# Kernel optimization log

Measured on AMD Instinct MI355X. Metric: run time of the kernel, lower is better.

Reference implementation:

```python
import jax, jax.numpy as jnp
import numpy as np

B, C, H, W = 16, 256, 56, 56
WH, WW = 7, 7
NH = 8            # heads
HID = 1024        # mlp hidden = int(4*dim)
N = WH * WW
EPS = 1e-5


def _rel_index():
    # mirrors the torch buffer computation in Rel_Attention.__init__
    coords = np.stack(np.meshgrid(np.arange(WH), np.arange(WW), indexing='ij')).reshape(2, -1)  # (2, N)
    rel = coords[:, :, None] - coords[:, None, :]  # (2, N, N)
    rel[0] += WH - 1
    rel[1] += WW - 1
    rel[0] *= 2 * WW - 1
    return jnp.asarray(rel.sum(0).reshape(-1))  # (N*N,)

REL_IDX = _rel_index()


def channel_ln(x, w, b):
    # LayerNorm over channel dim of NCHW tensor (permute -> LN -> permute back)
    xt = x.transpose(0, 2, 3, 1)  # BHWC
    mu = xt.mean(-1, keepdims=True)
    var = xt.var(-1, keepdims=True)
    xt = (xt - mu) / jnp.sqrt(var + EPS) * w + b
    return xt.transpose(0, 3, 1, 2)


def to_blocks(x):
    # (B,C,H,W) -> (B, H/wh, W/ww, C, wh, ww)
    b, c, h, w = x.shape
    x = x.reshape(b, c, h // WH, WH, w // WW, WW)
    return x.transpose(0, 2, 4, 1, 3, 5)


def unblock(x):
    # faithful to original: reshape(B, C, Hb*win_W, Hb*win_W)  (square sizes)
    b, hb, wb, c, wh, ww = x.shape
    return x.transpose(0, 3, 1, 4, 2, 5).reshape(b, c, hb * ww, hb * ww)


def rel_attention(xw, qkv_w, qkv_b, proj_w, proj_b, table):
    b, hb, wb, c = xw.shape[:4]
    hd = c // NH
    scale = hd ** (-0.5)
    xf = xw.reshape(-1, c, N)                                  # (M, C, N)
    qkv = jnp.einsum('oc,mcn->mon', qkv_w, xf) + qkv_b[None, :, None]
    q, k, v = jnp.split(qkv, 3, axis=1)

    def heads(t):
        return t.reshape(-1, NH, hd, N).transpose(0, 1, 3, 2)  # (M, h, N, d)

    q, k, v = heads(q), heads(k), heads(v)
    bias = table[REL_IDX].reshape(N, N, NH).transpose(2, 0, 1)  # (h, N, N)
    attn = jnp.einsum('mhnd,mhkd->mhnk', q, k) * scale + bias
    attn = jax.nn.softmax(attn, axis=-1)
    o = jnp.einsum('mhnk,mhkd->mhnd', attn, v)                 # (M, h, N, d)
    o = o.transpose(0, 1, 3, 2).reshape(-1, c, N)              # (M, C, N)
    o = jnp.einsum('oc,mcn->mon', proj_w, o) + proj_b[None, :, None]
    return o.reshape(b, hb, wb, c, WH, WW)


def mlp(x, fc1_w, fc1_b, fc2_w, fc2_b):
    h = jnp.einsum('oc,bchw->bohw', fc1_w, x) + fc1_b[None, :, None, None]
    h = jax.nn.gelu(h, approximate=False)
    return jnp.einsum('oc,bchw->bohw', fc2_w, h) + fc2_b[None, :, None, None]


def setup_inputs() -> dict:
    key = jax.random.key(0)
    ks = jax.random.split(key, 8)
    s = 0.02
    return {
        'x': jax.random.normal(ks[0], (B, C, H, W), jnp.float32),
        'ln1_w': jnp.ones((C,), jnp.float32),
        'ln1_b': jnp.zeros((C,), jnp.float32),
        'ln2_w': jnp.ones((C,), jnp.float32),
        'ln2_b': jnp.zeros((C,), jnp.float32),
        'qkv_w': jax.random.normal(ks[1], (3 * C, C), jnp.float32) * s,
        'qkv_b': jnp.zeros((3 * C,), jnp.float32),
        'proj_w': jax.random.normal(ks[2], (C, C), jnp.float32) * s,
        'proj_b': jnp.zeros((C,), jnp.float32),
        'rel_bias_table': jax.random.normal(ks[3], ((2 * WH - 1) * (2 * WW - 1), NH), jnp.float32) * s,
        'fc1_w': jax.random.normal(ks[4], (HID, C), jnp.float32) * s,
        'fc1_b': jnp.zeros((HID,), jnp.float32),
        'fc2_w': jax.random.normal(ks[5], (C, HID), jnp.float32) * s,
        'fc2_b': jnp.zeros((C,), jnp.float32),
    }


def reference(x, ln1_w, ln1_b, ln2_w, ln2_b, qkv_w, qkv_b, proj_w, proj_b,
              rel_bias_table, fc1_w, fc1_b, fc2_w, fc2_b):
    out = to_blocks(channel_ln(x, ln1_w, ln1_b))
    out = rel_attention(out, qkv_w, qkv_b, proj_w, proj_b, rel_bias_table)
    # original applies attn a second time before unblocking
    out = rel_attention(out, qkv_w, qkv_b, proj_w, proj_b, rel_bias_table)
    x = x + unblock(out)
    x = x + mlp(channel_ln(x, ln2_w, ln2_b), fc1_w, fc1_b, fc2_w, fc2_b)
    return x
```

## Files before the change

### kernel.cpp

```cpp
#include <hip/hip_runtime.h>
#include <stdint.h>

typedef uint16_t u16;
typedef short bf16x4 __attribute__((ext_vector_type(4)));
typedef short bf16x8 __attribute__((ext_vector_type(8)));
typedef float f32x4 __attribute__((ext_vector_type(4)));

__device__ __forceinline__ float bf2f(u16 s) {
  union { unsigned int i; float f; } c; c.i = ((unsigned int)s) << 16; return c.f;
}
__device__ __forceinline__ u16 f2bf(float f) {
  union { float f; unsigned int i; } c; c.f = f;
  unsigned int u = c.i;
  u += 0x7FFFu + ((u >> 16) & 1u);
  return (u16)(u >> 16);
}
__device__ __forceinline__ f32x4 mfma16(bf16x8 a, bf16x8 b, f32x4 c) {
  return __builtin_amdgcn_mfma_f32_16x16x32_bf16(a, b, c, 0, 0, 0);
}
__device__ __forceinline__ int dtype_flag(const u16* ln1w_raw) { return ln1w_raw[0] == 0x3F80 ? 1 : 0; }
__device__ __forceinline__ float loadF(const void* p, size_t i, int flag) {
  return flag ? bf2f(((const u16*)p)[i]) : ((const float*)p)[i];
}

__device__ __forceinline__ int frag_idx8(int n, int c0, int qc) {
  return (n < 48) ? (((n >> 4) * 8 + c0) * 64 + (n & 15) + 16 * qc)
                  : (1536 + c0 * 4 + qc);
}

#define OFF_QKVW 0
#define OFF_QKVB 196608
#define OFF_PROJW 197376
#define OFF_PROJB 262912
#define OFF_REL 263168
#define OFF_FC1W 264520
#define OFF_FC1B 526664
#define OFF_FC2W 527688
#define OFF_FC2B 789832
#define OFF_LN1W 790088
#define OFF_LN1B 790344
#define OFF_LN2W 790600
#define OFF_LN2B 790856
#define WC_TOTAL 791112

__global__ __launch_bounds__(256) void k_convert(const u16* __restrict__ ln1w_raw,
    const void* qkvw, const void* qkvb, const void* projw, const void* projb,
    const void* rel, const void* fc1w, const void* fc1b, const void* fc2w, const void* fc2b,
    const void* ln1w, const void* ln1b, const void* ln2w, const void* ln2b,
    u16* __restrict__ dst) {
  const int flag = dtype_flag(ln1w_raw);
  int i = blockIdx.x * 256 + threadIdx.x;
  if (i >= WC_TOTAL) return;
  const void* src; int off;
  if      (i < OFF_QKVB)  { src = qkvw;  off = i - OFF_QKVW; }
  else if (i < OFF_PROJW) { src = qkvb;  off = i - OFF_QKVB; }
  else if (i < OFF_PROJB) { src = projw; off = i - OFF_PROJW; }
  else if (i < OFF_REL)   { src = projb; off = i - OFF_PROJB; }
  else if (i < OFF_FC1W)  { src = rel;   off = i - OFF_REL; }
  else if (i < OFF_FC1B)  { src = fc1w;  off = i - OFF_FC1W; }
  else if (i < OFF_FC2W)  { src = fc1b;  off = i - OFF_FC1B; }
  else if (i < OFF_FC2B)  { src = fc2w;  off = i - OFF_FC2W; }
  else if (i < OFF_LN1W)  { src = fc2b;  off = i - OFF_FC2B; }
  else if (i < OFF_LN1B)  { src = ln1w;  off = i - OFF_LN1W; }
  else if (i < OFF_LN2W)  { src = ln1b;  off = i - OFF_LN1B; }
  else if (i < OFF_LN2B)  { src = ln2w;  off = i - OFF_LN2W; }
  else                    { src = ln2b;  off = i - OFF_LN2B; }
  if (i < OFF_QKVB) {
    int j = off & 7, li = (off >> 3) & 63, c0i = (off >> 9) & 7, grp = off >> 12;
    off = (grp * 16 + (li & 15)) * 256 + c0i * 32 + (li >> 4) * 8 + j;
  } else if (i >= OFF_PROJW && i < OFF_PROJB) {
    int j = off & 7, li = (off >> 3) & 63, c0i = (off >> 9) & 7, grp = off >> 12;
    off = (grp * 16 + (li & 15)) * 256 + c0i * 32 + (li >> 4) * 8 + j;
  } else if (i >= OFF_FC1W && i < OFF_FC1B) {
    int j = off & 7, li = (off >> 3) & 63, hj = (off >> 9) & 1, c0i = (off >> 10) & 7,
        w = (off >> 13) & 3, ch = off >> 15;
    off = (ch * 128 + w * 32 + hj * 16 + (li & 15)) * 256 + c0i * 32 + (li >> 4) * 8 + j;
  } else if (i >= OFF_FC2W && i < OFF_FC2B) {
    int j = off & 7, li = (off >> 3) & 63, oct = (off >> 9) & 3, kki = (off >> 11) & 3,
        ch = (off >> 13) & 7, w = off >> 16;
    off = (w * 64 + oct * 16 + (li & 15)) * 1024 + ch * 128 + kki * 32 + (li >> 4) * 8 + j;
  }
  dst[i] = flag ? ((const u16*)src)[off] : f2bf(((const float*)src)[off]);
}

__global__ __launch_bounds__(256) void k_ln1b(const void* __restrict__ xin,
                                              const u16* __restrict__ ln1w_raw,
                                              const u16* __restrict__ lw,
                                              const u16* __restrict__ lb,
                                              u16* __restrict__ win) {
  const int flag = dtype_flag(ln1w_raw);
  __shared__ float tile[56 * 257];
  __shared__ float smu[56], srs[56];
  const int bid = blockIdx.x;
  const int b = bid / 56, h = bid - b * 56;
  const int t = threadIdx.x;
  const int hb = h / 7, ph = h - hb * 7;
  if (!flag) {
#pragma unroll
    for (int i = 0; i < 14; ++i) {
      int chunk = i * 256 + t;
      int c = chunk / 14, w4 = (chunk - c * 14) * 4;
      const float* xp4 = (const float*)xin + ((size_t)(b * 256 + c) * 56 + h) * 56 + w4;
      f32x4 v = *(const f32x4*)xp4;
#pragma unroll
      for (int k = 0; k < 4; ++k) tile[(w4 + k) * 257 + c] = v[k];
    }
  } else {
#pragma unroll
    for (int i = 0; i < 7; ++i) {
      int chunk = i * 256 + t;
      int c = chunk / 7, w8 = (chunk - c * 7) * 8;
      const u16* xp8 = (const u16*)xin + ((size_t)(b * 256 + c) * 56 + h) * 56 + w8;
      bf16x8 v = *(const bf16x8*)xp8;
#pragma unroll
      for (int k = 0; k < 8; ++k) tile[(w8 + k) * 257 + c] = bf2f((u16)v[k]);
    }
  }
  __syncthreads();
  {
    const int row = t >> 2, qq = t & 3;
    float s = 0.f, q = 0.f;
    if (row < 56) {
      const float* tr = &tile[row * 257 + qq];
#pragma unroll 8
      for (int c0 = 0; c0 < 64; ++c0) { float v = tr[c0 * 4]; s += v; q += v * v; }
    }
    s += __shfl_xor(s, 1, 64); q += __shfl_xor(q, 1, 64);
    s += __shfl_xor(s, 2, 64); q += __shfl_xor(q, 2, 64);
    if (row < 56 && qq == 0) {
      float mm = s * (1.f / 256.f);
      float var = q * (1.f / 256.f) - mm * mm;
      smu[row] = mm; srs[row] = rsqrtf(var + 1e-5f);
    }
  }
  __syncthreads();
#pragma unroll
  for (int i = 0; i < 7; ++i) {
    int eid8 = i * 256 + t;
    int wp = eid8 >> 5, c8 = (eid8 & 31) << 3;
    const float mm = smu[wp], rs = srs[wp];
    const int m = b * 64 + hb * 8 + (wp / 7), n = ph * 7 + (wp % 7);
    bf16x8 o;
#pragma unroll
    for (int j = 0; j < 8; ++j) {
      int c = c8 + j;
      o[j] = (short)f2bf((tile[wp * 257 + c] - mm) * rs * bf2f(lw[c]) + bf2f(lb[c]));
    }
    const int idx8 = frag_idx8(n, c8 >> 5, (c8 >> 3) & 3);
    *(bf16x8*)&win[(size_t)m * 12544 + idx8 * 8] = o;
  }
}

__global__ __launch_bounds__(512) void k_attn_stage(const u16* __restrict__ win,
                                                    const u16* __restrict__ qkvw,
                                                    const u16* __restrict__ qkvb,
                                                    const u16* __restrict__ rel,
                                                    const u16* __restrict__ projw,
                                                    const u16* __restrict__ projb,
                                                    u16* __restrict__ wout,
                                                    int out_frag) {
  __shared__ __align__(16) u16 xs[12544];
  __shared__ __align__(16) u16 wa[8][7424];
  const int m = blockIdx.x;
  const int t = threadIdx.x;
  const int w = t >> 6, li = t & 63, lane = li & 15, quad = li >> 4;
  const int hg = w;
  const f32x4 z = {0.f, 0.f, 0.f, 0.f};
  const u16* src = win + (size_t)m * 12544;
#pragma unroll
  for (int i = 0; i < 4; ++i) {
    int chunk = i * 512 + t;
    if (chunk < 1568) *(bf16x8*)&xs[chunk * 8] = *(const bf16x8*)&src[(size_t)chunk * 8];
  }
  u16* qw = wa[w];
  u16* kw = wa[w] + 2560;
  u16* vw = wa[w] + 5120;
  u16* Pw = wa[w];
  u16* Ow = wa[w];
  for (int i = li; i < 15 * 40; i += 64) { qw[49 * 40 + i] = 0; kw[49 * 40 + i] = 0; }
  for (int i = li; i < 32 * 15; i += 64) { int d = i / 15, jn = i - d * 15; vw[d * 72 + 49 + jn] = 0; }
  __syncthreads();
  const float SCALE = 0.17677669529663687f;
  auto xfrag = [&](int nt, int c0i) -> bf16x8 {
    int idx8 = (nt < 3) ? ((nt * 8 + c0i) * 64 + li) : (1536 + c0i * 4 + quad);
    return *(const bf16x8*)&xs[idx8 * 8];
  };
#pragma unroll
  for (int part = 0; part < 2; ++part) {
    const int obase = part * 256 + hg * 32;
    f32x4 acc[4][2];
#pragma unroll
    for (int i = 0; i < 4; ++i) { acc[i][0] = z; acc[i][1] = z; }
#pragma unroll
    for (int c0i = 0; c0i < 8; ++c0i) {
      bf16x8 a[4], b[2];
#pragma unroll
      for (int nt = 0; nt < 4; ++nt) a[nt] = xfrag(nt, c0i);
#pragma unroll
      for (int oj = 0; oj < 2; ++oj)
        b[oj] = *(const bf16x8*)&qkvw[(size_t)(((part * 16 + hg * 2 + oj) * 8 + c0i) * 64 + li) * 8];
      __builtin_amdgcn_s_setprio(1);
#pragma unroll
      for (int nt = 0; nt < 4; ++nt)
#pragma unroll
        for (int oj = 0; oj < 2; ++oj) acc[nt][oj] = mfma16(a[nt], b[oj], acc[nt][oj]);
      __builtin_amdgcn_s_setprio(0);
    }
    u16* dstL = part ? kw : qw;
#pragma unroll
    for (int oj = 0; oj < 2; ++oj) {
      const int d = oj * 16 + lane;
      const float bias = bf2f(qkvb[obase + d]);
#pragma unroll
      for (int nt = 0; nt < 4; ++nt)
#pragma unroll
        for (int r = 0; r < 4; ++r) {
          int n = nt * 16 + quad * 4 + r;
          if (n < 49) dstL[n * 40 + d] = f2bf(acc[nt][oj][r] + bias);
        }
    }
  }
  {
    f32x4 acc[2][4];
#pragma unroll
    for (int i = 0; i < 2; ++i)
#pragma unroll
      for (int j = 0; j < 4; ++j) acc[i][j] = z;
#pragma unroll
    for (int c0i = 0; c0i < 8; ++c0i) {
      bf16x8 a[2], b[4];
#pragma unroll
      for (int vj = 0; vj < 2; ++vj)
        a[vj] = *(const bf16x8*)&qkvw[(size_t)(((32 + hg * 2 + vj) * 8 + c0i) * 64 + li) * 8];
#pragma unroll
      for (int nt = 0; nt < 4; ++nt) b[nt] = xfrag(nt, c0i);
      __builtin_amdgcn_s_setprio(1);
#pragma unroll
      for (int vj = 0; vj < 2; ++vj)
#pragma unroll
        for (int nt = 0; nt < 4; ++nt) acc[vj][nt] = mfma16(a[vj], b[nt], acc[vj][nt]);
      __builtin_amdgcn_s_setprio(0);
    }
#pragma unroll
    for (int vj = 0; vj < 2; ++vj)
#pragma unroll
      for (int r = 0; r < 4; ++r) {
        const int d = vj * 16 + quad * 4 + r;
        const float bias = bf2f(qkvb[512 + hg * 32 + d]);
#pragma unroll
        for (int nt = 0; nt < 4; ++nt) {
          int n = nt * 16 + lane;
          if (n < 49) vw[d * 72 + n] = f2bf(acc[vj][nt][r] + bias);
        }
      }
  }
  f32x4 s[4][4];
  {
    bf16x8 aq[4], bk[4];
#pragma unroll
    for (int nt = 0; nt < 4; ++nt) {
      aq[nt] = *(const bf16x8*)&qw[(nt * 16 + lane) * 40 + quad * 8];
      bk[nt] = *(const bf16x8*)&kw[(nt * 16 + lane) * 40 + quad * 8];
    }
    __builtin_amdgcn_s_setprio(1);
#pragma unroll
    for (int i = 0; i < 4; ++i)
#pragma unroll
      for (int j = 0; j < 4; ++j) s[i][j] = mfma16(aq[i], bk[j], z);
    __builtin_amdgcn_s_setprio(0);
  }
#pragma unroll
  for (int nt1 = 0; nt1 < 4; ++nt1) {
#pragma unroll
    for (int r = 0; r < 4; ++r) {
      int n1 = nt1 * 16 + quad * 4 + r;
      int n1c = n1 < 49 ? n1 : 48;
      int ph1 = n1c / 7, pw1 = n1c - ph1 * 7;
#pragma unroll
      for (int j = 0; j < 4; ++j) {
        int n2 = j * 16 + lane;
        float e;
        if (n2 < 49) {
          int ph2 = n2 / 7, pw2 = n2 - ph2 * 7;
          int idx = (ph1 - ph2 + 6) * 13 + (pw1 - pw2 + 6);
          e = __expf(s[nt1][j][r] * SCALE + bf2f(rel[idx * 8 + hg]));
        } else e = 0.f;
        Pw[n1 * 72 + j * 16 + lane] = f2bf(e);
      }
    }
  }
  {
    f32x4 o[4][2], ssum[4];
#pragma unroll
    for (int i = 0; i < 4; ++i) { o[i][0] = z; o[i][1] = z; ssum[i] = z; }
    bf16x8 bones;
#pragma unroll
    for (int k = 0; k < 8; ++k) bones[k] = (short)0x3F80;
#pragma unroll
    for (int kc = 0; kc < 2; ++kc) {
      bf16x8 ap[4], bv[2];
#pragma unroll
      for (int nt1 = 0; nt1 < 4; ++nt1)
        ap[nt1] = *(const bf16x8*)&Pw[(nt1 * 16 + lane) * 72 + kc * 32 + quad * 8];
#pragma unroll
      for (int dt = 0; dt < 2; ++dt)
        bv[dt] = *(const bf16x8*)&vw[(dt * 16 + lane) * 72 + kc * 32 + quad * 8];
      __builtin_amdgcn_s_setprio(1);
#pragma unroll
      for (int nt1 = 0; nt1 < 4; ++nt1) {
        ssum[nt1] = mfma16(ap[nt1], bones, ssum[nt1]);
#pragma unroll
        for (int dt = 0; dt < 2; ++dt) o[nt1][dt] = mfma16(ap[nt1], bv[dt], o[nt1][dt]);
      }
      __builtin_amdgcn_s_setprio(0);
    }
#pragma unroll
    for (int nt1 = 0; nt1 < 4; ++nt1) {
      f32x4 rv;
#pragma unroll
      for (int r = 0; r < 4; ++r) rv[r] = __builtin_amdgcn_rcpf(ssum[nt1][r]);
#pragma unroll
      for (int dt = 0; dt < 2; ++dt)
#pragma unroll
        for (int r = 0; r < 4; ++r) {
          int n1 = nt1 * 16 + quad * 4 + r;
          if (n1 < 49) Ow[n1 * 40 + dt * 16 + lane] = f2bf(o[nt1][dt][r] * rv[r]);
        }
    }
  }
  __syncthreads();
  {
    f32x4 acc[4][2];
#pragma unroll
    for (int i = 0; i < 4; ++i) { acc[i][0] = z; acc[i][1] = z; }
#pragma unroll
    for (int c0i = 0; c0i < 8; ++c0i) {
      bf16x8 a[4], b[2];
#pragma unroll
      for (int nt = 0; nt < 4; ++nt)
        a[nt] = *(const bf16x8*)&wa[c0i][(nt * 16 + lane) * 40 + quad * 8];
#pragma unroll
      for (int oj = 0; oj < 2; ++oj)
        b[oj] = *(const bf16x8*)&projw[(size_t)(((w * 2 + oj) * 8 + c0i) * 64 + li) * 8];
      __builtin_amdgcn_s_setprio(1);
#pragma unroll
      for (int nt = 0; nt < 4; ++nt)
#pragma unroll
        for (int oj = 0; oj < 2; ++oj) acc[nt][oj] = mfma16(a[nt], b[oj], acc[nt][oj]);
      __builtin_amdgcn_s_setprio(0);
    }
#pragma unroll
    for (int oj = 0; oj < 2; ++oj) {
      const int oc = w * 32 + oj * 16 + lane;
      const float bias = bf2f(projb[oc]);
#pragma unroll
      for (int nt = 0; nt < 4; ++nt)
#pragma unroll
        for (int r = 0; r < 4; ++r) {
          int n = nt * 16 + quad * 4 + r;
          if (n < 49) {
            u16 val = f2bf(acc[nt][oj][r] + bias);
            if (!out_frag) {
              wout[(size_t)m * 12544 + n * 256 + oc] = val;
            } else {
              int idx8 = frag_idx8(n, oc >> 5, (oc >> 3) & 3);
              wout[(size_t)m * 12544 + idx8 * 8 + (oc & 7)] = val;
            }
          }
        }
    }
  }
}

__global__ __launch_bounds__(256) void k_resid2(const void* __restrict__ xin,
                                                const u16* __restrict__ ln1w_raw,
                                                const u16* __restrict__ attn,
                                                const u16* __restrict__ l2w,
                                                const u16* __restrict__ l2b,
                                                u16* __restrict__ xrn,
                                                u16* __restrict__ ln2d) {
  const int flag = dtype_flag(ln1w_raw);
  __shared__ float tile[56 * 257];
  __shared__ float smu[56], srs[56];
  const int bid = blockIdx.x;
  const int b = bid / 56, h = bid - b * 56;
  const int t = threadIdx.x;
  const int hb = h / 7, ph = h - hb * 7;
#pragma unroll
  for (int i = 0; i < 7; ++i) {
    int eid8 = i * 256 + t;
    int wp = eid8 >> 5, c8 = (eid8 & 31) << 3;
    int mm = b * 64 + hb * 8 + (wp / 7), nn = ph * 7 + (wp % 7);
    bf16x8 v = *(const bf16x8*)&attn[(size_t)mm * 12544 + nn * 256 + c8];
    float* dst = &tile[wp * 257 + c8];
#pragma unroll
    for (int j = 0; j < 8; ++j) dst[j] = bf2f((u16)v[j]);
  }
  __syncthreads();
  if (!flag) {
#pragma unroll
    for (int i = 0; i < 14; ++i) {
      int chunk = i * 256 + t;
      int c = chunk / 14, w4 = (chunk - c * 14) * 4;
      const size_t base = ((size_t)(b * 256 + c) * 56 + h) * 56 + w4;
      f32x4 xv = *(const f32x4*)((const float*)xin + base);
      bf16x4 o4;
#pragma unroll
      for (int k = 0; k < 4; ++k) {
        float v = tile[(w4 + k) * 257 + c] + xv[k];
        tile[(w4 + k) * 257 + c] = v;
        o4[k] = (short)f2bf(v);
      }
      *(bf16x4*)&xrn[base] = o4;
    }
  } else {
#pragma unroll
    for (int i = 0; i < 7; ++i) {
      int chunk = i * 256 + t;
      int c = chunk / 7, w8 = (chunk - c * 7) * 8;
      const size_t base = ((size_t)(b * 256 + c) * 56 + h) * 56 + w8;
      bf16x8 xv = *(const bf16x8*)((const u16*)xin + base);
      bf16x8 o8;
#pragma unroll
      for (int k = 0; k < 8; ++k) {
        float v = tile[(w8 + k) * 257 + c] + bf2f((u16)xv[k]);
        tile[(w8 + k) * 257 + c] = v;
        o8[k] = (short)f2bf(v);
      }
      *(bf16x8*)&xrn[base] = o8;
    }
  }
  __syncthreads();
  {
    const int row = t >> 2, qq = t & 3;
    float s = 0.f, q = 0.f;
    if (row < 56) {
      const float* tr = &tile[row * 257 + qq];
#pragma unroll 8
      for (int c0 = 0; c0 < 64; ++c0) { float v = tr[c0 * 4]; s += v; q += v * v; }
    }
    s += __shfl_xor(s, 1, 64); q += __shfl_xor(q, 1, 64);
    s += __shfl_xor(s, 2, 64); q += __shfl_xor(q, 2, 64);
    if (row < 56 && qq == 0) {
      float mm = s * (1.f / 256.f);
      float var = q * (1.f / 256.f) - mm * mm;
      smu[row] = mm; srs[row] = rsqrtf(var + 1e-5f);
    }
  }
  __syncthreads();
#pragma unroll
  for (int i = 0; i < 7; ++i) {
    int eid8 = i * 256 + t;
    int wp = eid8 >> 5, c8 = (eid8 & 31) << 3;
    const float mm = smu[wp], rs = srs[wp];
    bf16x8 o;
#pragma unroll
    for (int j = 0; j < 8; ++j) {
      int c = c8 + j;
      o[j] = (short)f2bf((tile[wp * 257 + c] - mm) * rs * bf2f(l2w[c]) + bf2f(l2b[c]));
    }
    const int p = b * 3136 + h * 56 + wp;
    const int pblk = p >> 6, pt = (p & 63) >> 4, r16 = p & 15;
    const int c0i = c8 >> 5, quad = (c8 >> 3) & 3;
    *(bf16x8*)&ln2d[(size_t)((((pblk * 4 + pt) * 8 + c0i) * 64 + quad * 16 + r16)) << 3] = o;
  }
}

__global__ __launch_bounds__(256, 3) void k_mlp2(const u16* __restrict__ aG,
                                                 const u16* __restrict__ w1,
                                                 const u16* __restrict__ b1,
                                                 const u16* __restrict__ w2,
                                                 const u16* __restrict__ b2,
                                                 const u16* __restrict__ xrn,
                                                 const u16* __restrict__ ln1w_raw,
                                                 void* __restrict__ out) {
  const int flag = dtype_flag(ln1w_raw);
  __shared__ __align__(16) u16 arena[25088];
  u16* xp = arena;
  u16* g  = arena + 16384;
  const int pblk = blockIdx.x;
  const int pix0 = pblk * 64;
  const int t = threadIdx.x;
  const int w = t >> 6, li = t & 63, lane = li & 15, quad = li >> 4;
  {
    const u16* asrc = aG + (size_t)pblk * 16384;
#pragma unroll
    for (int i = 0; i < 8; ++i) {
      int idx = i * 256 + t;
      *(bf16x8*)&xp[idx * 8] = *(const bf16x8*)&asrc[(size_t)idx * 8];
    }
  }
  __syncthreads();
  const f32x4 z = {0.f, 0.f, 0.f, 0.f};
  f32x4 acc2[4][4];
#pragma unroll
  for (int i = 0; i < 4; ++i)
#pragma unroll
    for (int j = 0; j < 4; ++j) acc2[i][j] = z;

  auto fc1 = [&](int ch) {
    f32x4 a1[4][2];
#pragma unroll
    for (int i = 0; i < 4; ++i) { a1[i][0] = z; a1[i][1] = z; }
#pragma unroll
    for (int c0i = 0; c0i < 8; ++c0i) {
      bf16x8 av[4], bw[2];
#pragma unroll
      for (int pt = 0; pt < 4; ++pt)
        av[pt] = *(const bf16x8*)&xp[((pt * 8 + c0i) * 64 + li) * 8];
#pragma unroll
      for (int hj = 0; hj < 2; ++hj)
        bw[hj] = *(const bf16x8*)&w1[(size_t)((((ch * 4 + w) * 8 + c0i) * 2 + hj) * 64 + li) * 8];
#pragma unroll
      for (int pt = 0; pt < 4; ++pt)
#pragma unroll
        for (int hj = 0; hj < 2; ++hj) a1[pt][hj] = mfma16(av[pt], bw[hj], a1[pt][hj]);
    }
#pragma unroll
    for (int hj = 0; hj < 2; ++hj) {
      const int hl = w * 32 + hj * 16 + lane;
      const float bias = bf2f(b1[ch * 128 + hl]);
#pragma unroll
      for (int pt = 0; pt < 4; ++pt)
#pragma unroll
        for (int r = 0; r < 4; ++r) {
          float u_ = a1[pt][hj][r] + bias;
          float y = u_ * fmaf(u_ * u_, 0.035677408136300125f, 0.7978845608028654f);
          float e2 = __expf(-2.f * y);
          float v = u_ * __builtin_amdgcn_rcpf(1.f + e2);
          g[(pt * 16 + quad * 4 + r) * 136 + hl] = f2bf(v);
        }
    }
  };
  auto fc2 = [&](int ch) {
#pragma unroll
    for (int kki = 0; kki < 4; ++kki) {
      bf16x8 aw[4], bg[4];
#pragma unroll
      for (int oct = 0; oct < 4; ++oct)
        aw[oct] = *(const bf16x8*)&w2[(size_t)((((w * 8 + ch) * 4 + kki) * 4 + oct) * 64 + li) * 8];
#pragma unroll
      for (int pt = 0; pt < 4; ++pt)
        bg[pt] = *(const bf16x8*)&g[(pt * 16 + lane) * 136 + kki * 32 + quad * 8];
#pragma unroll
      for (int oct = 0; oct < 4; ++oct)
#pragma unroll
        for (int pt = 0; pt < 4; ++pt) acc2[oct][pt] = mfma16(aw[oct], bg[pt], acc2[oct][pt]);
    }
  };

  fc1(0);
  __syncthreads();
#pragma unroll 1
  for (int ch = 0; ch < 8; ++ch) {
    fc2(ch);
    if (ch < 7) {
      __syncthreads();
      fc1(ch + 1);
      __syncthreads();
    }
  }

  float* Ob = (float*)arena;
  const int b_ = pix0 / 3136, rem0 = pix0 - b_ * 3136;
  const int sub = t & 7, r0 = t >> 3;
#pragma unroll 1
  for (int e = 0; e < 2; ++e) {
    __syncthreads();
    if ((w >> 1) == e) {
      const int wl = w & 1;
#pragma unroll
      for (int oct = 0; oct < 4; ++oct)
#pragma unroll
        for (int pt = 0; pt < 4; ++pt)
#pragma unroll
          for (int r = 0; r < 4; ++r)
            Ob[(wl * 64 + oct * 16 + quad * 4 + r) * 65 + pt * 16 + lane] = acc2[oct][pt][r];
    }
    __syncthreads();
    bf16x8 xr[4];
    size_t addrs[4];
#pragma unroll
    for (int i = 0; i < 4; ++i) {
      const int oc = e * 128 + i * 32 + r0;
      addrs[i] = (size_t)(b_ * 256 + oc) * 3136 + rem0 + sub * 8;
      xr[i] = *(const bf16x8*)&xrn[addrs[i]];
    }
#pragma unroll
    for (int i = 0; i < 4; ++i) {
      const int oc = e * 128 + i * 32 + r0;
      const float bias = bf2f(b2[oc]);
      const float* obr = &Ob[(i * 32 + r0) * 65 + sub * 8];
      float v[8];
#pragma unroll
      for (int j = 0; j < 8; ++j)
        v[j] = obr[j] + bias + bf2f((u16)xr[i][j]);
      if (flag) {
        bf16x8 o8;
#pragma unroll
        for (int j = 0; j < 8; ++j) o8[j] = (short)f2bf(v[j]);
        *(bf16x8*)&((u16*)out)[addrs[i]] = o8;
      } else {
        float* dst = &((float*)out)[addrs[i]];
        f32x4 lo = {v[0], v[1], v[2], v[3]}, hi = {v[4], v[5], v[6], v[7]};
        *(f32x4*)&dst[0] = lo;
        *(f32x4*)&dst[4] = hi;
      }
    }
  }
}

extern "C" void kernel_launch(void* const* d_in, const int* in_sizes, int n_in,
                              void* d_out, int out_size, void* d_ws, size_t ws_size,
                              hipStream_t stream) {
  (void)in_sizes; (void)n_in; (void)out_size; (void)ws_size;
  const void* x     = d_in[0];
  const u16* ln1w_raw = (const u16*)d_in[1];
  u16* ws = (u16*)d_ws;
  const size_t R = 12845056;
  u16* R0 = ws;
  u16* R1 = ws + R;
  u16* R2 = ws + 2 * R;
  u16* WC = ws + 3 * R;
  const u16* qkvw_c = WC + OFF_QKVW;
  const u16* qkvb_c = WC + OFF_QKVB;
  const u16* projw_c = WC + OFF_PROJW;
  const u16* projb_c = WC + OFF_PROJB;
  const u16* rel_c  = WC + OFF_REL;
  const u16* fc1w_c = WC + OFF_FC1W;
  const u16* fc1b_c = WC + OFF_FC1B;
  const u16* fc2w_c = WC + OFF_FC2W;
  const u16* fc2b_c = WC + OFF_FC2B;
  const u16* ln1w_c = WC + OFF_LN1W;
  const u16* ln1b_c = WC + OFF_LN1B;
  const u16* ln2w_c = WC + OFF_LN2W;
  const u16* ln2b_c = WC + OFF_LN2B;

  k_convert<<<(WC_TOTAL + 255) / 256, 256, 0, stream>>>(
      ln1w_raw, d_in[5], d_in[6], d_in[7], d_in[8], d_in[9],
      d_in[10], d_in[11], d_in[12], d_in[13], d_in[1], d_in[2], d_in[3], d_in[4], WC);

  k_ln1b      <<<896, 256, 0, stream>>>(x, ln1w_raw, ln1w_c, ln1b_c, R0);
  k_attn_stage<<<1024, 512, 0, stream>>>(R0, qkvw_c, qkvb_c, rel_c, projw_c, projb_c, R1, 1);
  k_attn_stage<<<1024, 512, 0, stream>>>(R1, qkvw_c, qkvb_c, rel_c, projw_c, projb_c, R2, 0);
  k_resid2    <<<896, 256, 0, stream>>>(x, ln1w_raw, R2, ln2w_c, ln2b_c, R0, R1);
  k_mlp2      <<<784, 256, 0, stream>>>(R1, fc1w_c, fc1b_c, fc2w_c, fc2b_c, R0, ln1w_raw, d_out);
}
```

Before: 426.6 us.

## Keep MLP input tile in registers, transpose rel-bias table, add MFMA priority hints

In the fused MLP kernel, each wave now loads its A-operand fragments (the normalized 64-pixel tile) straight from global memory into 32 bf16x8 registers. This replaces staging them in LDS, which shrinks shared memory and drops a barrier and the per-chunk LDS reads. In exchange, register pressure rises by 128 VGPRs under a 3-blocks-per-CU launch bound, so spills are possible. The relative-position bias table is re-laid out head-major during weight prep, so attention computes the bias address as a simple difference of precomputed bases. s_setprio hints are also added around the MFMA bursts.

```diff
diff --git a/kernel.cpp b/kernel.cpp
--- a/kernel.cpp
+++ b/kernel.cpp
@@ -71,6 +71,9 @@
   } else if (i >= OFF_PROJW && i < OFF_PROJB) {
     int j = off & 7, li = (off >> 3) & 63, c0i = (off >> 9) & 7, grp = off >> 12;
     off = (grp * 16 + (li & 15)) * 256 + c0i * 32 + (li >> 4) * 8 + j;
+  } else if (i >= OFF_REL && i < OFF_FC1W) {
+    int hg_ = off / 169, idx_ = off - hg_ * 169;
+    off = idx_ * 8 + hg_;
   } else if (i >= OFF_FC1W && i < OFF_FC1B) {
     int j = off & 7, li = (off >> 3) & 63, hj = (off >> 9) & 1, c0i = (off >> 10) & 7,
         w = (off >> 13) & 3, ch = off >> 15;
@@ -269,23 +272,29 @@
       for (int j = 0; j < 4; ++j) s[i][j] = mfma16(aq[i], bk[j], z);
     __builtin_amdgcn_s_setprio(0);
   }
-#pragma unroll
-  for (int nt1 = 0; nt1 < 4; ++nt1) {
-#pragma unroll
-    for (int r = 0; r < 4; ++r) {
-      int n1 = nt1 * 16 + quad * 4 + r;
-      int n1c = n1 < 49 ? n1 : 48;
-      int ph1 = n1c / 7, pw1 = n1c - ph1 * 7;
-#pragma unroll
-      for (int j = 0; j < 4; ++j) {
-        int n2 = j * 16 + lane;
-        float e;
-        if (n2 < 49) {
-          int ph2 = n2 / 7, pw2 = n2 - ph2 * 7;
-          int idx = (ph1 - ph2 + 6) * 13 + (pw1 - pw2 + 6);
-          e = __expf(s[nt1][j][r] * SCALE + bf2f(rel[idx * 8 + hg]));
-        } else e = 0.f;
-        Pw[n1 * 72 + j * 16 + lane] = f2bf(e);
+  {
+    const u16* relh = rel + hg * 169 + 84;
+    int b2j[4]; bool v2j[4];
+#pragma unroll
+    for (int j = 0; j < 4; ++j) {
+      int n2 = j * 16 + lane;
+      v2j[j] = (n2 < 49);
+      int p2 = n2 / 7;
+      b2j[j] = p2 * 13 + (n2 - p2 * 7);
+    }
+#pragma unroll
+    for (int nt1 = 0; nt1 < 4; ++nt1) {
+#pragma unroll
+      for (int r = 0; r < 4; ++r) {
+        int n1 = nt1 * 16 + quad * 4 + r;
+        int n1c = n1 < 49 ? n1 : 48;
+        int p1 = n1c / 7;
+        int base1 = p1 * 13 + (n1c - p1 * 7);
+#pragma unroll
+        for (int j = 0; j < 4; ++j) {
+          float e = v2j[j] ? __expf(s[nt1][j][r] * SCALE + bf2f(relh[base1 - b2j[j]])) : 0.f;
+          Pw[n1 * 72 + j * 16 + lane] = f2bf(e);
+        }
       }
     }
   }
@@ -475,22 +484,21 @@
                                                  const u16* __restrict__ ln1w_raw,
                                                  void* __restrict__ out) {
   const int flag = dtype_flag(ln1w_raw);
-  __shared__ __align__(16) u16 arena[25088];
-  u16* xp = arena;
-  u16* g  = arena + 16384;
+  __shared__ __align__(16) u16 arena[16640];
+  u16* g = arena;
   const int pblk = blockIdx.x;
   const int pix0 = pblk * 64;
   const int t = threadIdx.x;
   const int w = t >> 6, li = t & 63, lane = li & 15, quad = li >> 4;
+  bf16x8 xpr[8][4];
   {
     const u16* asrc = aG + (size_t)pblk * 16384;
 #pragma unroll
-    for (int i = 0; i < 8; ++i) {
-      int idx = i * 256 + t;
-      *(bf16x8*)&xp[idx * 8] = *(const bf16x8*)&asrc[(size_t)idx * 8];
-    }
-  }
-  __syncthreads();
+    for (int c0i = 0; c0i < 8; ++c0i)
+#pragma unroll
+      for (int pt = 0; pt < 4; ++pt)
+        xpr[c0i][pt] = *(const bf16x8*)&asrc[(size_t)((pt * 8 + c0i) * 64 + li) * 8];
+  }
   const f32x4 z = {0.f, 0.f, 0.f, 0.f};
   f32x4 acc2[4][4];
 #pragma unroll
@@ -504,17 +512,16 @@
     for (int i = 0; i < 4; ++i) { a1[i][0] = z; a1[i][1] = z; }
 #pragma unroll
     for (int c0i = 0; c0i < 8; ++c0i) {
-      bf16x8 av[4], bw[2];
-#pragma unroll
-      for (int pt = 0; pt < 4; ++pt)
-        av[pt] = *(const bf16x8*)&xp[((pt * 8 + c0i) * 64 + li) * 8];
+      bf16x8 bw[2];
 #pragma unroll
       for (int hj = 0; hj < 2; ++hj)
         bw[hj] = *(const bf16x8*)&w1[(size_t)((((ch * 4 + w) * 8 + c0i) * 2 + hj) * 64 + li) * 8];
+      __builtin_amdgcn_s_setprio(1);
 #pragma unroll
       for (int pt = 0; pt < 4; ++pt)
 #pragma unroll
-        for (int hj = 0; hj < 2; ++hj) a1[pt][hj] = mfma16(av[pt], bw[hj], a1[pt][hj]);
+        for (int hj = 0; hj < 2; ++hj) a1[pt][hj] = mfma16(xpr[c0i][pt], bw[hj], a1[pt][hj]);
+      __builtin_amdgcn_s_setprio(0);
     }
 #pragma unroll
     for (int hj = 0; hj < 2; ++hj) {
@@ -542,10 +549,12 @@
 #pragma unroll
       for (int pt = 0; pt < 4; ++pt)
         bg[pt] = *(const bf16x8*)&g[(pt * 16 + lane) * 136 + kki * 32 + quad * 8];
+      __builtin_amdgcn_s_setprio(1);
 #pragma unroll
       for (int oct = 0; oct < 4; ++oct)
 #pragma unroll
         for (int pt = 0; pt < 4; ++pt) acc2[oct][pt] = mfma16(aw[oct], bg[pt], acc2[oct][pt]);
+      __builtin_amdgcn_s_setprio(0);
     }
   };
 
```

Result: slower. 486.1 us (+13.9%).
